# Optimization experiments

Measured on AMD Instinct MI355X. Metric: run time of the kernel, lower is better.

The kernel has to match this reference:

```python
import jax, jax.numpy as jnp
import numpy as np

N_NODES = 50000
N_GRAPHS = 512
HIDDEN = 128
BN_EPS = 1e-5


def setup_inputs() -> dict:
    key = jax.random.key(0)
    ks = jax.random.split(key, 16)
    E = 800000
    x = jax.random.normal(ks[0], (N_NODES, 1), dtype=jnp.float32)
    pos = jax.random.normal(ks[1], (N_NODES, 3), dtype=jnp.float32)
    edge_index = jax.random.randint(ks[2], (2, E), 0, N_NODES, dtype=jnp.int64)
    batch = jnp.sort(jax.random.randint(ks[3], (N_NODES,), 0, N_GRAPHS, dtype=jnp.int64))

    def lin(k, fan_in, fan_out):
        bound = 1.0 / np.sqrt(fan_in)
        return jax.random.uniform(k, (fan_in, fan_out), jnp.float32, -bound, bound)

    # conv1: in=1 -> concat dim 2*1+3=5
    c1_w1 = lin(ks[4], 5, HIDDEN); c1_b1 = jnp.zeros((HIDDEN,), jnp.float32)
    c1_w2 = lin(ks[5], HIDDEN, HIDDEN); c1_b2 = jnp.zeros((HIDDEN,), jnp.float32)
    # conv2: in=128 -> concat dim 2*128+3=259
    c2_w1 = lin(ks[6], 2 * HIDDEN + 3, HIDDEN); c2_b1 = jnp.zeros((HIDDEN,), jnp.float32)
    c2_w2 = lin(ks[7], HIDDEN, HIDDEN); c2_b2 = jnp.zeros((HIDDEN,), jnp.float32)
    # predictor MLP [128, 128, 1], bias=[False, True], batch_norm + relu between
    p_w1 = lin(ks[8], HIDDEN, HIDDEN)
    bn_gamma = jnp.ones((HIDDEN,), jnp.float32)
    bn_beta = jnp.zeros((HIDDEN,), jnp.float32)
    p_w2 = lin(ks[9], HIDDEN, 1)
    p_b2 = jnp.zeros((1,), jnp.float32)
    return {
        "x": x, "pos": pos, "edge_index": edge_index, "batch": batch,
        "c1_w1": c1_w1, "c1_b1": c1_b1, "c1_w2": c1_w2, "c1_b2": c1_b2,
        "c2_w1": c2_w1, "c2_b1": c2_b1, "c2_w2": c2_w2, "c2_b2": c2_b2,
        "p_w1": p_w1, "bn_gamma": bn_gamma, "bn_beta": bn_beta,
        "p_w2": p_w2, "p_b2": p_b2,
    }


def _conv(x, pos, src, dst, w1, b1, w2, b2):
    # gather endpoints; PyG: x_j = x[src], x_i = x[dst], aggregate into dst
    feat = jnp.concatenate([x[dst], x[src], pos[src] - pos[dst]], axis=-1)  # [E, 2F+3]
    msg = jax.nn.relu(feat @ w1 + b1) @ w2 + b2  # [E, H]
    return jax.ops.segment_sum(msg, dst, num_segments=N_NODES)  # [N, H]


def reference(x, pos, edge_index, batch,
              c1_w1, c1_b1, c1_w2, c1_b2,
              c2_w1, c2_b1, c2_w2, c2_b2,
              p_w1, bn_gamma, bn_beta, p_w2, p_b2):
    src, dst = edge_index[0], edge_index[1]
    h = jax.nn.relu(_conv(x, pos, src, dst, c1_w1, c1_b1, c1_w2, c1_b2))
    h = jax.nn.relu(_conv(h, pos, src, dst, c2_w1, c2_b1, c2_w2, c2_b2))
    g = jax.ops.segment_sum(h, batch, num_segments=N_GRAPHS)  # [G, H] global add pool
    # predictor: Linear(no bias) -> BatchNorm(train stats) -> ReLU -> Linear(bias)
    z = g @ p_w1
    mean = jnp.mean(z, axis=0)
    var = jnp.var(z, axis=0)
    z = bn_gamma * (z - mean) * jax.lax.rsqrt(var + BN_EPS) + bn_beta
    z = jax.nn.relu(z)
    return z @ p_w2 + p_b2  # [G, 1]
```

## Files before the change

### kernel.cpp

```cpp
#include <hip/hip_runtime.h>
#include <hip/hip_bf16.h>

#define HID 128
#define DMAX 64

typedef unsigned int uint;
typedef unsigned short ushort;
using short8 = __attribute__((ext_vector_type(8))) short;
using f32x4  = __attribute__((ext_vector_type(4))) float;

#define MFMA_B16(a, b, c) __builtin_amdgcn_mfma_f32_16x16x32_bf16(a, b, c, 0, 0, 0)

__device__ inline ushort bf16rn(float f) {
  uint u = __float_as_uint(f);
  u += 0x7fff + ((u >> 16) & 1);
  return (ushort)(u >> 16);
}
__device__ inline uint packbf(float a, float b) {
  return (uint)bf16rn(a) | ((uint)bf16rn(b) << 16);
}
__device__ inline float bflo(uint u) { return __uint_as_float(u << 16); }
__device__ inline float bfhi(uint u) { return __uint_as_float(u & 0xffff0000u); }

__global__ __launch_bounds__(256) void k_prep(
    const float* __restrict__ x, const float* __restrict__ pos,
    const float* __restrict__ c1w2, const float* __restrict__ c2w1, const float* __restrict__ c2w2,
    float4* __restrict__ xp, int* __restrict__ deg, float* __restrict__ g,
    ushort* __restrict__ w1t, ushort* __restrict__ wdt,
    ushort* __restrict__ wst, ushort* __restrict__ w2t,
    int N, int G, int Npad) {
  int idx = blockIdx.x * 256 + threadIdx.x;
  if (idx < Npad) deg[idx] = 0;
  if (idx < G * HID) g[idx] = 0.f;
  if (idx < N) {
    xp[idx] = make_float4(pos[3 * idx], pos[3 * idx + 1], pos[3 * idx + 2], x[idx]);
  }
  {
    int m = idx >> 14, e = idx & 16383;
    int c = e >> 7, k = e & 127;
    const float* src;
    ushort* dst;
    if (m == 0)      { src = c1w2;              dst = w1t; }
    else if (m == 1) { src = c2w1;              dst = wdt; }
    else if (m == 2) { src = c2w1 + 128 * 128;  dst = wst; }
    else             { src = c2w2;              dst = w2t; }
    dst[e] = bf16rn(src[k * 128 + c]);
  }
}

__global__ void k_build(const int* __restrict__ dstv, const int* __restrict__ srcv,
                        int* __restrict__ deg, int* __restrict__ srcsP, int E) {
  int e = blockIdx.x * 256 + threadIdx.x;
  if (e < E) {
    int d = dstv[e];
    int r = atomicAdd(&deg[d], 1);
    if (r < DMAX) srcsP[(size_t)d * DMAX + r] = srcv[e];
  }
}

__global__ __launch_bounds__(64) void k_conv1(
    const float4* __restrict__ xp,
    const int* __restrict__ deg, const int* __restrict__ srcsP,
    const float* __restrict__ w1, const float* __restrict__ b1, uint* __restrict__ hs) {
  int n = blockIdx.x;
  int lane = threadIdx.x;
  int f0 = 2 * lane;
  __shared__ float sxs[64];
  __shared__ float sdp[3][64];
  int cnt = min(deg[n], DMAX);
  float4 me = xp[n];
  float xi = me.w;
  float2 a1 = *(const float2*)&w1[HID + f0];
  float2 a2 = *(const float2*)&w1[2 * HID + f0];
  float2 a3 = *(const float2*)&w1[3 * HID + f0];
  float2 a4 = *(const float2*)&w1[4 * HID + f0];
  float c_0 = fmaf(xi, w1[f0],     b1[f0]);
  float c_1 = fmaf(xi, w1[f0 + 1], b1[f0 + 1]);
  float acc0 = 0.f, acc1 = 0.f;
  if (lane < cnt) {
    int s = srcsP[(size_t)n * DMAX + lane];
    float4 v = xp[s];
    sxs[lane] = v.w;
    sdp[0][lane] = v.x - me.x;
    sdp[1][lane] = v.y - me.y;
    sdp[2][lane] = v.z - me.z;
  }
  __syncthreads();
  for (int k = 0; k < cnt; ++k) {
    float xj = sxs[k], d0 = sdp[0][k], d1 = sdp[1][k], d2 = sdp[2][k];
    float h0 = fmaf(xj, a1.x, fmaf(d0, a2.x, fmaf(d1, a3.x, fmaf(d2, a4.x, c_0))));
    float h1 = fmaf(xj, a1.y, fmaf(d0, a2.y, fmaf(d1, a3.y, fmaf(d2, a4.y, c_1))));
    acc0 += fmaxf(h0, 0.f);
    acc1 += fmaxf(h1, 0.f);
  }
  hs[(size_t)n * 64 + lane] = packbf(acc0, acc1);
}

__global__ __launch_bounds__(64) void k_conv2(
    const float4* __restrict__ xp,
    const int* __restrict__ deg, const int* __restrict__ srcsP,
    const float* __restrict__ pd, const uint* __restrict__ ps,
    const float* __restrict__ wc, uint* __restrict__ hs) {
  int n = blockIdx.x;
  int lane = threadIdx.x;
  int eg = lane >> 4;
  int fb = lane & 15;
  int f0 = 8 * fb;
  __shared__ int ssrc[64];
  __shared__ float sdp[3][64];
  int cnt = min(deg[n], DMAX);
  float4 me = xp[n];
  float c0[8], c1[8], c2[8], pdv[8], acc[8];
  #pragma unroll
  for (int i = 0; i < 8; ++i) {
    c0[i]  = wc[f0 + i];
    c1[i]  = wc[HID + f0 + i];
    c2[i]  = wc[2 * HID + f0 + i];
    pdv[i] = pd[(size_t)n * HID + f0 + i];
    acc[i] = 0.f;
  }
  if (lane < cnt) {
    int s = srcsP[(size_t)n * DMAX + lane];
    float4 v = xp[s];
    ssrc[lane] = s;
    sdp[0][lane] = v.x - me.x;
    sdp[1][lane] = v.y - me.y;
    sdp[2][lane] = v.z - me.z;
  }
  __syncthreads();
  for (int k = 0; k < cnt; k += 16) {
    int ke[4] = {k + eg, k + 4 + eg, k + 8 + eg, k + 12 + eg};
    int kc[4];
    #pragma unroll
    for (int j = 0; j < 4; ++j) kc[j] = min(ke[j], cnt - 1);
    int se[4] = {ssrc[kc[0]], ssrc[kc[1]], ssrc[kc[2]], ssrc[kc[3]]};
    uint4 u[4];
    #pragma unroll
    for (int j = 0; j < 4; ++j) u[j] = *(const uint4*)&ps[(size_t)se[j] * 64 + fb * 4];
    #pragma unroll
    for (int j = 0; j < 4; ++j) {
      float d0 = sdp[0][kc[j]], d1 = sdp[1][kc[j]], d2 = sdp[2][kc[j]];
      bool vv = ke[j] < cnt;
      uint uu[4] = {u[j].x, u[j].y, u[j].z, u[j].w};
      if (vv) {
        #pragma unroll
        for (int q = 0; q < 4; ++q) {
          float w0  = pdv[2*q]   + fmaf(d0, c0[2*q],   fmaf(d1, c1[2*q],   d2 * c2[2*q]));
          float w1v = pdv[2*q+1] + fmaf(d0, c0[2*q+1], fmaf(d1, c1[2*q+1], d2 * c2[2*q+1]));
          acc[2*q]   += fmaxf(w0  + bflo(uu[q]), 0.f);
          acc[2*q+1] += fmaxf(w1v + bfhi(uu[q]), 0.f);
        }
      }
    }
  }
  #pragma unroll
  for (int i = 0; i < 8; ++i) {
    acc[i] += __shfl_xor(acc[i], 16);
    acc[i] += __shfl_xor(acc[i], 32);
  }
  if (eg == 0) {
    uint4 o;
    o.x = packbf(acc[0], acc[1]);
    o.y = packbf(acc[2], acc[3]);
    o.z = packbf(acc[4], acc[5]);
    o.w = packbf(acc[6], acc[7]);
    *(uint4*)&hs[(size_t)n * 64 + fb * 4] = o;
  }
}

template <int MODE>
__global__ __launch_bounds__(256) void k_mgemm(
    const ushort* __restrict__ A, const ushort* __restrict__ Wt, const ushort* __restrict__ Wt2,
    const float* __restrict__ bias, const int* __restrict__ deg, const int* __restrict__ batch,
    uint* __restrict__ Obf, float* __restrict__ Of, int M) {
  int t = threadIdx.x;
  int l = t & 63;
  int rl = l & 15, kg = l >> 4;
  int r = blockIdx.x * 64 + (t >> 6) * 16 + rl;
  int rc = min(r, M - 1);
  bool valid = (r < M);
  const short8* arow = (const short8*)(A + (size_t)rc * 128);
  short8 af0 = arow[kg], af1 = arow[4 + kg], af2 = arow[8 + kg], af3 = arow[12 + kg];
  float dg = 0.f;
  int bt = 0, gf = 0, gl = 0;
  if (MODE == 0 || MODE == 2) dg = valid ? (float)deg[r] : 0.f;
  if (MODE == 2) {
    bt = batch[rc];
    gf = __shfl(bt, 0);
    gl = __shfl(bt, 15);
  }
  #pragma unroll
  for (int nt = 0; nt < 8; ++nt) {
    const short8* wrow = (const short8*)(Wt + (size_t)(nt * 16 + rl) * 128);
    f32x4 acc = {0.f, 0.f, 0.f, 0.f};
    acc = MFMA_B16(wrow[kg],      af0, acc);
    acc = MFMA_B16(wrow[4 + kg],  af1, acc);
    acc = MFMA_B16(wrow[8 + kg],  af2, acc);
    acc = MFMA_B16(wrow[12 + kg], af3, acc);
    int c0 = nt * 16 + kg * 4;
    if (MODE == 0) {
      f32x4 b4 = *(const f32x4*)&bias[c0];
      float v0 = fmaxf(fmaf(dg, b4[0], acc[0]), 0.f);
      float v1 = fmaxf(fmaf(dg, b4[1], acc[1]), 0.f);
      float v2 = fmaxf(fmaf(dg, b4[2], acc[2]), 0.f);
      float v3 = fmaxf(fmaf(dg, b4[3], acc[3]), 0.f);
      if (valid) {
        uint2 o = {packbf(v0, v1), packbf(v2, v3)};
        *(uint2*)&Obf[(size_t)r * 64 + (c0 >> 1)] = o;
      }
    } else if (MODE == 1) {
      const short8* w2row = (const short8*)(Wt2 + (size_t)(nt * 16 + rl) * 128);
      f32x4 acc2 = {0.f, 0.f, 0.f, 0.f};
      acc2 = MFMA_B16(w2row[kg],      af0, acc2);
      acc2 = MFMA_B16(w2row[4 + kg],  af1, acc2);
      acc2 = MFMA_B16(w2row[8 + kg],  af2, acc2);
      acc2 = MFMA_B16(w2row[12 + kg], af3, acc2);
      if (valid) {
        f32x4 b4 = *(const f32x4*)&bias[c0];
        f32x4 pdv = {acc[0] + b4[0], acc[1] + b4[1], acc[2] + b4[2], acc[3] + b4[3]};
        *(f32x4*)&Of[(size_t)r * 128 + c0] = pdv;
        uint2 o = {packbf(acc2[0], acc2[1]), packbf(acc2[2], acc2[3])};
        *(uint2*)&Obf[(size_t)r * 64 + (c0 >> 1)] = o;
      }
    } else {
      f32x4 b4 = *(const f32x4*)&bias[c0];
      float v0 = valid ? fmaxf(fmaf(dg, b4[0], acc[0]), 0.f) : 0.f;
      float v1 = valid ? fmaxf(fmaf(dg, b4[1], acc[1]), 0.f) : 0.f;
      float v2 = valid ? fmaxf(fmaf(dg, b4[2], acc[2]), 0.f) : 0.f;
      float v3 = valid ? fmaxf(fmaf(dg, b4[3], acc[3]), 0.f) : 0.f;
      for (int gg = gf; gg <= gl; ++gg) {
        bool mine = (bt == gg);
        float s0 = mine ? v0 : 0.f;
        float s1 = mine ? v1 : 0.f;
        float s2 = mine ? v2 : 0.f;
        float s3 = mine ? v3 : 0.f;
        #pragma unroll
        for (int m = 1; m <= 8; m <<= 1) {
          s0 += __shfl_xor(s0, m);
          s1 += __shfl_xor(s1, m);
          s2 += __shfl_xor(s2, m);
          s3 += __shfl_xor(s3, m);
        }
        if (rl == 0) {
          float* gp = &Of[(size_t)gg * 128 + c0];
          atomicAdd(gp + 0, s0);
          atomicAdd(gp + 1, s1);
          atomicAdd(gp + 2, s2);
          atomicAdd(gp + 3, s3);
        }
      }
    }
  }
}

__global__ __launch_bounds__(256) void k_pgemm(
    const float* __restrict__ A, const float* __restrict__ W, float* __restrict__ O1, int M) {
  __shared__ float As[128][36];
  int t = threadIdx.x;
  int n0 = blockIdx.x * 32;
  int j = t & 127, m = t >> 7;
  for (int idx = t; idx < 32 * 128; idx += 256) {
    int r = idx >> 7, i = idx & 127;
    int n = n0 + r;
    As[i][r] = (n < M) ? A[(size_t)n * 128 + i] : 0.f;
  }
  __syncthreads();
  float acc[16];
  #pragma unroll
  for (int r = 0; r < 16; ++r) acc[r] = 0.f;
  int rb = m * 16;
  for (int i = 0; i < 128; ++i) {
    float w = W[i * 128 + j];
    const float4* ap = reinterpret_cast<const float4*>(&As[i][rb]);
    #pragma unroll
    for (int q = 0; q < 4; ++q) {
      float4 a = ap[q];
      acc[q * 4 + 0] = fmaf(a.x, w, acc[q * 4 + 0]);
      acc[q * 4 + 1] = fmaf(a.y, w, acc[q * 4 + 1]);
      acc[q * 4 + 2] = fmaf(a.z, w, acc[q * 4 + 2]);
      acc[q * 4 + 3] = fmaf(a.w, w, acc[q * 4 + 3]);
    }
  }
  #pragma unroll
  for (int r = 0; r < 16; ++r) {
    int n = n0 + rb + r;
    if (n < M) O1[(size_t)n * 128 + j] = acc[r];
  }
}

__global__ __launch_bounds__(256) void k_bn2(const float* __restrict__ z,
                                             float* __restrict__ mv, int G) {
  int j = blockIdx.x;
  int t = threadIdx.x;
  float v1 = (t < G) ? z[(size_t)t * 128 + j] : 0.f;
  float v2 = (t + 256 < G) ? z[(size_t)(t + 256) * 128 + j] : 0.f;
  float s = v1 + v2;
  float q = fmaf(v1, v1, v2 * v2);
  #pragma unroll
  for (int off = 32; off; off >>= 1) {
    s += __shfl_down(s, off);
    q += __shfl_down(q, off);
  }
  __shared__ float ws[4], wq[4];
  int wid = t >> 6, lane = t & 63;
  if (lane == 0) { ws[wid] = s; wq[wid] = q; }
  __syncthreads();
  if (t == 0) {
    float S = ws[0] + ws[1] + ws[2] + ws[3];
    float Q = wq[0] + wq[1] + wq[2] + wq[3];
    float mean = S / (float)G;
    float var = Q / (float)G - mean * mean;
    mv[j] = mean;
    mv[128 + j] = rsqrtf(var + 1e-5f);
  }
}

__global__ __launch_bounds__(256) void k_final(
    const float* __restrict__ z, const float* __restrict__ mv,
    const float* __restrict__ gamma, const float* __restrict__ beta,
    const float* __restrict__ w2, const float* __restrict__ b2,
    float* __restrict__ out, int G) {
  int wid = threadIdx.x >> 6, lane = threadIdx.x & 63;
  int r = blockIdx.x * 4 + wid;
  if (r >= G) return;
  float acc = 0.f;
  #pragma unroll
  for (int h = 0; h < 2; ++h) {
    int jj = lane + h * 64;
    float v = z[(size_t)r * 128 + jj];
    float zn = fmaf((v - mv[jj]) * mv[128 + jj], gamma[jj], beta[jj]);
    acc = fmaf(fmaxf(zn, 0.f), w2[jj], acc);
  }
  #pragma unroll
  for (int off = 32; off; off >>= 1) acc += __shfl_down(acc, off);
  if (lane == 0) out[r] = acc + b2[0];
}

extern "C" void kernel_launch(void* const* d_in, const int* in_sizes, int n_in,
                              void* d_out, int out_size, void* d_ws, size_t ws_size,
                              hipStream_t stream) {
  const float* x     = (const float*)d_in[0];
  const float* pos   = (const float*)d_in[1];
  const int*   eidx  = (const int*)d_in[2];
  const int*   batch = (const int*)d_in[3];
  const float* c1w1  = (const float*)d_in[4];
  const float* c1b1  = (const float*)d_in[5];
  const float* c1w2  = (const float*)d_in[6];
  const float* c1b2  = (const float*)d_in[7];
  const float* c2w1  = (const float*)d_in[8];
  const float* c2b1  = (const float*)d_in[9];
  const float* c2w2  = (const float*)d_in[10];
  const float* c2b2  = (const float*)d_in[11];
  const float* pw1   = (const float*)d_in[12];
  const float* gamma = (const float*)d_in[13];
  const float* beta  = (const float*)d_in[14];
  const float* pw2   = (const float*)d_in[15];
  const float* pb2   = (const float*)d_in[16];
  (void)n_in; (void)ws_size;

  const int N = in_sizes[0];
  const int E = in_sizes[2] / 2;
  const int G = out_size;
  const int* srcv = eidx;
  const int* dstv = eidx + E;

  char* w = (char*)d_ws;
  size_t o = 0;
  auto carve = [&](size_t bytes) { void* p = w + o; o = (o + bytes + 255) & ~(size_t)255; return p; };
  int Npad = ((N + 255) / 256) * 256;
  int* deg    = (int*)carve((size_t)Npad * 4);
  int* srcsP  = (int*)carve((size_t)N * DMAX * 4);
  float4* xp  = (float4*)carve((size_t)N * 16);
  uint*   hs1  = (uint*)carve((size_t)N * 64 * 4);
  ushort* h1   = (ushort*)carve((size_t)N * 128 * 2);
  float*  pdf  = (float*)carve((size_t)N * 128 * 4);
  uint*   psb  = (uint*)carve((size_t)N * 64 * 4);
  uint*   hs2  = (uint*)carve((size_t)N * 64 * 4);
  ushort* w1t  = (ushort*)carve(16384 * 2);
  ushort* wdt  = (ushort*)carve(16384 * 2);
  ushort* wst  = (ushort*)carve(16384 * 2);
  ushort* w2t  = (ushort*)carve(16384 * 2);
  float* g    = (float*)carve((size_t)G * HID * 4);
  float* z    = (float*)carve((size_t)G * HID * 4);
  float* mv   = (float*)carve(256 * 4);

  int nbE = (E + 255) / 256;

  k_prep<<<256, 256, 0, stream>>>(x, pos, c1w2, c2w1, c2w2,
                                  xp, deg, g, w1t, wdt, wst, w2t, N, G, Npad);
  k_build<<<nbE, 256, 0, stream>>>(dstv, srcv, deg, srcsP, E);

  int gb = (N + 63) / 64;
  k_conv1<<<N, 64, 0, stream>>>(xp, deg, srcsP, c1w1, c1b1, hs1);
  k_mgemm<0><<<gb, 256, 0, stream>>>((const ushort*)hs1, w1t, nullptr, c1b2, deg, nullptr,
                                     (uint*)h1, nullptr, N);
  k_mgemm<1><<<gb, 256, 0, stream>>>(h1, wdt, wst, c2b1, nullptr, nullptr,
                                     psb, pdf, N);
  k_conv2<<<N, 64, 0, stream>>>(xp, deg, srcsP, pdf, psb, c2w1 + 256 * HID, hs2);
  k_mgemm<2><<<gb, 256, 0, stream>>>((const ushort*)hs2, w2t, nullptr, c2b2, deg, batch,
                                     nullptr, g, N);
  k_pgemm<<<(G + 31) / 32, 256, 0, stream>>>(g, pw1, z, G);
  k_bn2<<<HID, 256, 0, stream>>>(z, mv, G);
  k_final<<<(G + 3) / 4, 256, 0, stream>>>(z, mv, gamma, beta, pw2, pb2, (float*)d_out, G);
}
```

Measured before the change: 206.7 us.

## Split degree atomics into two parity buckets and store pd as bf16

Edges are split by index parity into two counter arrays and two 32-slot halves of each adjacency row. This halves atomic contention on popular destination nodes during the CSR build. The conv2 precomputed dst-term is now written and read as bf16 rather than fp32, cutting that buffer's traffic. The changes add precision loss on pd, and each half now overflows separately at 32 entries instead of the row overflowing at 64.

```diff
diff --git a/kernel.cpp b/kernel.cpp
--- a/kernel.cpp
+++ b/kernel.cpp
@@ -3,6 +3,7 @@
 
 #define HID 128
 #define DMAX 64
+#define BCAP 32
 
 typedef unsigned int uint;
 typedef unsigned short ushort;
@@ -25,12 +26,15 @@
 __global__ __launch_bounds__(256) void k_prep(
     const float* __restrict__ x, const float* __restrict__ pos,
     const float* __restrict__ c1w2, const float* __restrict__ c2w1, const float* __restrict__ c2w2,
-    float4* __restrict__ xp, int* __restrict__ deg, float* __restrict__ g,
+    float4* __restrict__ xp, int* __restrict__ deg2, float* __restrict__ g,
     ushort* __restrict__ w1t, ushort* __restrict__ wdt,
     ushort* __restrict__ wst, ushort* __restrict__ w2t,
     int N, int G, int Npad) {
   int idx = blockIdx.x * 256 + threadIdx.x;
-  if (idx < Npad) deg[idx] = 0;
+  if (idx < Npad) {
+    deg2[idx] = 0;
+    deg2[Npad + idx] = 0;
+  }
   if (idx < G * HID) g[idx] = 0.f;
   if (idx < N) {
     xp[idx] = make_float4(pos[3 * idx], pos[3 * idx + 1], pos[3 * idx + 2], x[idx]);
@@ -49,25 +53,28 @@
 }
 
 __global__ void k_build(const int* __restrict__ dstv, const int* __restrict__ srcv,
-                        int* __restrict__ deg, int* __restrict__ srcsP, int E) {
+                        int* __restrict__ deg2, int* __restrict__ srcsP, int E, int Npad) {
   int e = blockIdx.x * 256 + threadIdx.x;
   if (e < E) {
     int d = dstv[e];
-    int r = atomicAdd(&deg[d], 1);
-    if (r < DMAX) srcsP[(size_t)d * DMAX + r] = srcv[e];
+    int b = e & 1;
+    int r = atomicAdd(&deg2[(size_t)b * Npad + d], 1);
+    if (r < BCAP) srcsP[(size_t)d * DMAX + b * BCAP + r] = srcv[e];
   }
 }
 
 __global__ __launch_bounds__(64) void k_conv1(
     const float4* __restrict__ xp,
-    const int* __restrict__ deg, const int* __restrict__ srcsP,
-    const float* __restrict__ w1, const float* __restrict__ b1, uint* __restrict__ hs) {
+    const int* __restrict__ deg2, const int* __restrict__ srcsP,
+    const float* __restrict__ w1, const float* __restrict__ b1, uint* __restrict__ hs,
+    int Npad) {
   int n = blockIdx.x;
   int lane = threadIdx.x;
   int f0 = 2 * lane;
   __shared__ float sxs[64];
   __shared__ float sdp[3][64];
-  int cnt = min(deg[n], DMAX);
+  int d0 = min(deg2[n], BCAP);
+  int d1 = min(deg2[Npad + n], BCAP);
   float4 me = xp[n];
   float xi = me.w;
   float2 a1 = *(const float2*)&w1[HID + f0];
@@ -77,7 +84,8 @@
   float c_0 = fmaf(xi, w1[f0],     b1[f0]);
   float c_1 = fmaf(xi, w1[f0 + 1], b1[f0 + 1]);
   float acc0 = 0.f, acc1 = 0.f;
-  if (lane < cnt) {
+  bool valid = (lane < BCAP) ? (lane < d0) : (lane - BCAP < d1);
+  if (valid) {
     int s = srcsP[(size_t)n * DMAX + lane];
     float4 v = xp[s];
     sxs[lane] = v.w;
@@ -86,21 +94,26 @@
     sdp[2][lane] = v.z - me.z;
   }
   __syncthreads();
-  for (int k = 0; k < cnt; ++k) {
-    float xj = sxs[k], d0 = sdp[0][k], d1 = sdp[1][k], d2 = sdp[2][k];
-    float h0 = fmaf(xj, a1.x, fmaf(d0, a2.x, fmaf(d1, a3.x, fmaf(d2, a4.x, c_0))));
-    float h1 = fmaf(xj, a1.y, fmaf(d0, a2.y, fmaf(d1, a3.y, fmaf(d2, a4.y, c_1))));
-    acc0 += fmaxf(h0, 0.f);
-    acc1 += fmaxf(h1, 0.f);
+  #pragma unroll
+  for (int seg = 0; seg < 2; ++seg) {
+    int kb = seg * BCAP;
+    int kcnt = seg ? d1 : d0;
+    for (int k = kb; k < kb + kcnt; ++k) {
+      float xj = sxs[k], d0v = sdp[0][k], d1v = sdp[1][k], d2v = sdp[2][k];
+      float h0 = fmaf(xj, a1.x, fmaf(d0v, a2.x, fmaf(d1v, a3.x, fmaf(d2v, a4.x, c_0))));
+      float h1 = fmaf(xj, a1.y, fmaf(d0v, a2.y, fmaf(d1v, a3.y, fmaf(d2v, a4.y, c_1))));
+      acc0 += fmaxf(h0, 0.f);
+      acc1 += fmaxf(h1, 0.f);
+    }
   }
   hs[(size_t)n * 64 + lane] = packbf(acc0, acc1);
 }
 
 __global__ __launch_bounds__(64) void k_conv2(
     const float4* __restrict__ xp,
-    const int* __restrict__ deg, const int* __restrict__ srcsP,
-    const float* __restrict__ pd, const uint* __restrict__ ps,
-    const float* __restrict__ wc, uint* __restrict__ hs) {
+    const int* __restrict__ deg2, const int* __restrict__ srcsP,
+    const uint* __restrict__ pdb, const uint* __restrict__ ps,
+    const float* __restrict__ wc, uint* __restrict__ hs, int Npad) {
   int n = blockIdx.x;
   int lane = threadIdx.x;
   int eg = lane >> 4;
@@ -108,18 +121,26 @@
   int f0 = 8 * fb;
   __shared__ int ssrc[64];
   __shared__ float sdp[3][64];
-  int cnt = min(deg[n], DMAX);
+  int d0 = min(deg2[n], BCAP);
+  int d1 = min(deg2[Npad + n], BCAP);
   float4 me = xp[n];
   float c0[8], c1[8], c2[8], pdv[8], acc[8];
+  uint4 pdu = *(const uint4*)&pdb[(size_t)n * 64 + fb * 4];
+  uint pdua[4] = {pdu.x, pdu.y, pdu.z, pdu.w};
+  #pragma unroll
+  for (int i = 0; i < 4; ++i) {
+    pdv[2 * i]     = bflo(pdua[i]);
+    pdv[2 * i + 1] = bfhi(pdua[i]);
+  }
   #pragma unroll
   for (int i = 0; i < 8; ++i) {
     c0[i]  = wc[f0 + i];
     c1[i]  = wc[HID + f0 + i];
     c2[i]  = wc[2 * HID + f0 + i];
-    pdv[i] = pd[(size_t)n * HID + f0 + i];
     acc[i] = 0.f;
   }
-  if (lane < cnt) {
+  bool validl = (lane < BCAP) ? (lane < d0) : (lane - BCAP < d1);
+  if (validl) {
     int s = srcsP[(size_t)n * DMAX + lane];
     float4 v = xp[s];
     ssrc[lane] = s;
@@ -128,27 +149,32 @@
     sdp[2][lane] = v.z - me.z;
   }
   __syncthreads();
-  for (int k = 0; k < cnt; k += 16) {
-    int ke[4] = {k + eg, k + 4 + eg, k + 8 + eg, k + 12 + eg};
-    int kc[4];
-    #pragma unroll
-    for (int j = 0; j < 4; ++j) kc[j] = min(ke[j], cnt - 1);
-    int se[4] = {ssrc[kc[0]], ssrc[kc[1]], ssrc[kc[2]], ssrc[kc[3]]};
-    uint4 u[4];
-    #pragma unroll
-    for (int j = 0; j < 4; ++j) u[j] = *(const uint4*)&ps[(size_t)se[j] * 64 + fb * 4];
-    #pragma unroll
-    for (int j = 0; j < 4; ++j) {
-      float d0 = sdp[0][kc[j]], d1 = sdp[1][kc[j]], d2 = sdp[2][kc[j]];
-      bool vv = ke[j] < cnt;
-      uint uu[4] = {u[j].x, u[j].y, u[j].z, u[j].w};
-      if (vv) {
-        #pragma unroll
-        for (int q = 0; q < 4; ++q) {
-          float w0  = pdv[2*q]   + fmaf(d0, c0[2*q],   fmaf(d1, c1[2*q],   d2 * c2[2*q]));
-          float w1v = pdv[2*q+1] + fmaf(d0, c0[2*q+1], fmaf(d1, c1[2*q+1], d2 * c2[2*q+1]));
-          acc[2*q]   += fmaxf(w0  + bflo(uu[q]), 0.f);
-          acc[2*q+1] += fmaxf(w1v + bfhi(uu[q]), 0.f);
+  #pragma unroll
+  for (int seg = 0; seg < 2; ++seg) {
+    int kb = seg * BCAP;
+    int cnt = seg ? d1 : d0;
+    for (int k = 0; k < cnt; k += 16) {
+      int ke[4] = {k + eg, k + 4 + eg, k + 8 + eg, k + 12 + eg};
+      int kc[4];
+      #pragma unroll
+      for (int j = 0; j < 4; ++j) kc[j] = kb + min(ke[j], cnt - 1);
+      int se[4] = {ssrc[kc[0]], ssrc[kc[1]], ssrc[kc[2]], ssrc[kc[3]]};
+      uint4 u[4];
+      #pragma unroll
+      for (int j = 0; j < 4; ++j) u[j] = *(const uint4*)&ps[(size_t)se[j] * 64 + fb * 4];
+      #pragma unroll
+      for (int j = 0; j < 4; ++j) {
+        float dd0 = sdp[0][kc[j]], dd1 = sdp[1][kc[j]], dd2 = sdp[2][kc[j]];
+        bool vv = ke[j] < cnt;
+        uint uu[4] = {u[j].x, u[j].y, u[j].z, u[j].w};
+        if (vv) {
+          #pragma unroll
+          for (int q = 0; q < 4; ++q) {
+            float w0  = pdv[2*q]   + fmaf(dd0, c0[2*q],   fmaf(dd1, c1[2*q],   dd2 * c2[2*q]));
+            float w1v = pdv[2*q+1] + fmaf(dd0, c0[2*q+1], fmaf(dd1, c1[2*q+1], dd2 * c2[2*q+1]));
+            acc[2*q]   += fmaxf(w0  + bflo(uu[q]), 0.f);
+            acc[2*q+1] += fmaxf(w1v + bfhi(uu[q]), 0.f);
+          }
         }
       }
     }
@@ -171,8 +197,8 @@
 template <int MODE>
 __global__ __launch_bounds__(256) void k_mgemm(
     const ushort* __restrict__ A, const ushort* __restrict__ Wt, const ushort* __restrict__ Wt2,
-    const float* __restrict__ bias, const int* __restrict__ deg, const int* __restrict__ batch,
-    uint* __restrict__ Obf, float* __restrict__ Of, int M) {
+    const float* __restrict__ bias, const int* __restrict__ deg2, const int* __restrict__ batch,
+    uint* __restrict__ Obf, uint* __restrict__ Obf2, float* __restrict__ Of, int M, int Npad) {
   int t = threadIdx.x;
   int l = t & 63;
   int rl = l & 15, kg = l >> 4;
@@ -183,7 +209,7 @@
   short8 af0 = arow[kg], af1 = arow[4 + kg], af2 = arow[8 + kg], af3 = arow[12 + kg];
   float dg = 0.f;
   int bt = 0, gf = 0, gl = 0;
-  if (MODE == 0 || MODE == 2) dg = valid ? (float)deg[r] : 0.f;
+  if (MODE == 0 || MODE == 2) dg = valid ? (float)(deg2[r] + deg2[Npad + r]) : 0.f;
   if (MODE == 2) {
     bt = batch[rc];
     gf = __shfl(bt, 0);
@@ -217,10 +243,11 @@
       acc2 = MFMA_B16(w2row[12 + kg], af3, acc2);
       if (valid) {
         f32x4 b4 = *(const f32x4*)&bias[c0];
-        f32x4 pdv = {acc[0] + b4[0], acc[1] + b4[1], acc[2] + b4[2], acc[3] + b4[3]};
-        *(f32x4*)&Of[(size_t)r * 128 + c0] = pdv;
-        uint2 o = {packbf(acc2[0], acc2[1]), packbf(acc2[2], acc2[3])};
-        *(uint2*)&Obf[(size_t)r * 64 + (c0 >> 1)] = o;
+        uint2 opd = {packbf(acc[0] + b4[0], acc[1] + b4[1]),
+                     packbf(acc[2] + b4[2], acc[3] + b4[3])};
+        *(uint2*)&Obf2[(size_t)r * 64 + (c0 >> 1)] = opd;
+        uint2 ops = {packbf(acc2[0], acc2[1]), packbf(acc2[2], acc2[3])};
+        *(uint2*)&Obf[(size_t)r * 64 + (c0 >> 1)] = ops;
       }
     } else {
       f32x4 b4 = *(const f32x4*)&bias[c0];
@@ -368,12 +395,12 @@
   size_t o = 0;
   auto carve = [&](size_t bytes) { void* p = w + o; o = (o + bytes + 255) & ~(size_t)255; return p; };
   int Npad = ((N + 255) / 256) * 256;
-  int* deg    = (int*)carve((size_t)Npad * 4);
+  int* deg2   = (int*)carve((size_t)2 * Npad * 4);
   int* srcsP  = (int*)carve((size_t)N * DMAX * 4);
   float4* xp  = (float4*)carve((size_t)N * 16);
   uint*   hs1  = (uint*)carve((size_t)N * 64 * 4);
   ushort* h1   = (ushort*)carve((size_t)N * 128 * 2);
-  float*  pdf  = (float*)carve((size_t)N * 128 * 4);
+  uint*   pdb  = (uint*)carve((size_t)N * 64 * 4);
   uint*   psb  = (uint*)carve((size_t)N * 64 * 4);
   uint*   hs2  = (uint*)carve((size_t)N * 64 * 4);
   ushort* w1t  = (ushort*)carve(16384 * 2);
@@ -387,18 +414,18 @@
   int nbE = (E + 255) / 256;
 
   k_prep<<<256, 256, 0, stream>>>(x, pos, c1w2, c2w1, c2w2,
-                                  xp, deg, g, w1t, wdt, wst, w2t, N, G, Npad);
-  k_build<<<nbE, 256, 0, stream>>>(dstv, srcv, deg, srcsP, E);
+                                  xp, deg2, g, w1t, wdt, wst, w2t, N, G, Npad);
+  k_build<<<nbE, 256, 0, stream>>>(dstv, srcv, deg2, srcsP, E, Npad);
 
   int gb = (N + 63) / 64;
-  k_conv1<<<N, 64, 0, stream>>>(xp, deg, srcsP, c1w1, c1b1, hs1);
-  k_mgemm<0><<<gb, 256, 0, stream>>>((const ushort*)hs1, w1t, nullptr, c1b2, deg, nullptr,
-                                     (uint*)h1, nullptr, N);
+  k_conv1<<<N, 64, 0, stream>>>(xp, deg2, srcsP, c1w1, c1b1, hs1, Npad);
+  k_mgemm<0><<<gb, 256, 0, stream>>>((const ushort*)hs1, w1t, nullptr, c1b2, deg2, nullptr,
+                                     (uint*)h1, nullptr, nullptr, N, Npad);
   k_mgemm<1><<<gb, 256, 0, stream>>>(h1, wdt, wst, c2b1, nullptr, nullptr,
-                                     psb, pdf, N);
-  k_conv2<<<N, 64, 0, stream>>>(xp, deg, srcsP, pdf, psb, c2w1 + 256 * HID, hs2);
-  k_mgemm<2><<<gb, 256, 0, stream>>>((const ushort*)hs2, w2t, nullptr, c2b2, deg, batch,
-                                     nullptr, g, N);
+                                     psb, pdb, nullptr, N, Npad);
+  k_conv2<<<N, 64, 0, stream>>>(xp, deg2, srcsP, pdb, psb, c2w1 + 256 * HID, hs2, Npad);
+  k_mgemm<2><<<gb, 256, 0, stream>>>((const ushort*)hs2, w2t, nullptr, c2b2, deg2, batch,
+                                     nullptr, nullptr, g, N, Npad);
   k_pgemm<<<(G + 31) / 32, 256, 0, stream>>>(g, pw1, z, G);
   k_bn2<<<HID, 256, 0, stream>>>(z, mv, G);
   k_final<<<(G + 3) / 4, 256, 0, stream>>>(z, mv, gamma, beta, pw2, pb2, (float*)d_out, G);
```

New measurement: 211.1 us. 2.1% more time.

## Fuse conv1 output GEMM with conv2 projections and pad degree counters

Applied to the files above, without the earlier changes.

Merges the conv1 second-layer GEMM and the conv2 first-layer projections into one kernel that keeps the intermediate activations in LDS, removing a global round-trip and a launch. The dst-side projection is now stored as bf16 instead of fp32, halving its traffic at some precision cost. Degree counters are spread to one per 128-byte line to reduce atomic contention, at the cost of a larger buffer to zero and scattered degree reads.

```diff
diff --git a/kernel.cpp b/kernel.cpp
--- a/kernel.cpp
+++ b/kernel.cpp
@@ -3,6 +3,7 @@
 
 #define HID 128
 #define DMAX 64
+#define DSTRIDE 32
 
 typedef unsigned int uint;
 typedef unsigned short ushort;
@@ -25,12 +26,13 @@
 __global__ __launch_bounds__(256) void k_prep(
     const float* __restrict__ x, const float* __restrict__ pos,
     const float* __restrict__ c1w2, const float* __restrict__ c2w1, const float* __restrict__ c2w2,
-    float4* __restrict__ xp, int* __restrict__ deg, float* __restrict__ g,
+    float4* __restrict__ xp, int* __restrict__ degP, float* __restrict__ g,
     ushort* __restrict__ w1t, ushort* __restrict__ wdt,
     ushort* __restrict__ wst, ushort* __restrict__ w2t,
     int N, int G, int Npad) {
   int idx = blockIdx.x * 256 + threadIdx.x;
-  if (idx < Npad) deg[idx] = 0;
+  int stride = gridDim.x * 256;
+  for (int i = idx; i < Npad * DSTRIDE; i += stride) degP[i] = 0;
   if (idx < G * HID) g[idx] = 0.f;
   if (idx < N) {
     xp[idx] = make_float4(pos[3 * idx], pos[3 * idx + 1], pos[3 * idx + 2], x[idx]);
@@ -49,25 +51,25 @@
 }
 
 __global__ void k_build(const int* __restrict__ dstv, const int* __restrict__ srcv,
-                        int* __restrict__ deg, int* __restrict__ srcsP, int E) {
+                        int* __restrict__ degP, int* __restrict__ srcsP, int E) {
   int e = blockIdx.x * 256 + threadIdx.x;
   if (e < E) {
     int d = dstv[e];
-    int r = atomicAdd(&deg[d], 1);
+    int r = atomicAdd(&degP[(size_t)d * DSTRIDE], 1);
     if (r < DMAX) srcsP[(size_t)d * DMAX + r] = srcv[e];
   }
 }
 
 __global__ __launch_bounds__(64) void k_conv1(
     const float4* __restrict__ xp,
-    const int* __restrict__ deg, const int* __restrict__ srcsP,
+    const int* __restrict__ degP, const int* __restrict__ srcsP,
     const float* __restrict__ w1, const float* __restrict__ b1, uint* __restrict__ hs) {
   int n = blockIdx.x;
   int lane = threadIdx.x;
   int f0 = 2 * lane;
   __shared__ float sxs[64];
   __shared__ float sdp[3][64];
-  int cnt = min(deg[n], DMAX);
+  int cnt = min(degP[(size_t)n * DSTRIDE], DMAX);
   float4 me = xp[n];
   float xi = me.w;
   float2 a1 = *(const float2*)&w1[HID + f0];
@@ -96,10 +98,75 @@
   hs[(size_t)n * 64 + lane] = packbf(acc0, acc1);
 }
 
+__global__ __launch_bounds__(256) void k_mfuse(
+    const ushort* __restrict__ A, const ushort* __restrict__ W1t,
+    const ushort* __restrict__ Wdt, const ushort* __restrict__ Wst,
+    const float* __restrict__ b1, const float* __restrict__ bd,
+    const int* __restrict__ degP,
+    uint* __restrict__ psb, uint* __restrict__ pdb, int M) {
+  __shared__ uint hl[64][68];
+  int t = threadIdx.x;
+  int l = t & 63;
+  int rl = l & 15, kg = l >> 4, wv = t >> 6;
+  int rloc = wv * 16 + rl;
+  int r = blockIdx.x * 64 + rloc;
+  int rc = min(r, M - 1);
+  bool valid = (r < M);
+  const short8* arow = (const short8*)(A + (size_t)rc * 128);
+  short8 af0 = arow[kg], af1 = arow[4 + kg], af2 = arow[8 + kg], af3 = arow[12 + kg];
+  float dg = valid ? (float)degP[(size_t)r * DSTRIDE] : 0.f;
+  #pragma unroll
+  for (int nt = 0; nt < 8; ++nt) {
+    const short8* wrow = (const short8*)(W1t + (size_t)(nt * 16 + rl) * 128);
+    f32x4 acc = {0.f, 0.f, 0.f, 0.f};
+    acc = MFMA_B16(wrow[kg],      af0, acc);
+    acc = MFMA_B16(wrow[4 + kg],  af1, acc);
+    acc = MFMA_B16(wrow[8 + kg],  af2, acc);
+    acc = MFMA_B16(wrow[12 + kg], af3, acc);
+    int c0 = nt * 16 + kg * 4;
+    f32x4 b4 = *(const f32x4*)&b1[c0];
+    float v0 = fmaxf(fmaf(dg, b4[0], acc[0]), 0.f);
+    float v1 = fmaxf(fmaf(dg, b4[1], acc[1]), 0.f);
+    float v2 = fmaxf(fmaf(dg, b4[2], acc[2]), 0.f);
+    float v3 = fmaxf(fmaf(dg, b4[3], acc[3]), 0.f);
+    hl[rloc][(c0 >> 1)]     = packbf(v0, v1);
+    hl[rloc][(c0 >> 1) + 1] = packbf(v2, v3);
+  }
+  __syncthreads();
+  const uint* hrow = hl[rloc];
+  short8 bfrag[4];
+  #pragma unroll
+  for (int i = 0; i < 4; ++i) bfrag[i] = *(const short8*)&hrow[i * 16 + kg * 4];
+  #pragma unroll
+  for (int nt = 0; nt < 8; ++nt) {
+    const short8* wsrow = (const short8*)(Wst + (size_t)(nt * 16 + rl) * 128);
+    const short8* wdrow = (const short8*)(Wdt + (size_t)(nt * 16 + rl) * 128);
+    f32x4 accS = {0.f, 0.f, 0.f, 0.f};
+    f32x4 accD = {0.f, 0.f, 0.f, 0.f};
+    accS = MFMA_B16(wsrow[kg],      bfrag[0], accS);
+    accS = MFMA_B16(wsrow[4 + kg],  bfrag[1], accS);
+    accS = MFMA_B16(wsrow[8 + kg],  bfrag[2], accS);
+    accS = MFMA_B16(wsrow[12 + kg], bfrag[3], accS);
+    accD = MFMA_B16(wdrow[kg],      bfrag[0], accD);
+    accD = MFMA_B16(wdrow[4 + kg],  bfrag[1], accD);
+    accD = MFMA_B16(wdrow[8 + kg],  bfrag[2], accD);
+    accD = MFMA_B16(wdrow[12 + kg], bfrag[3], accD);
+    int c0 = nt * 16 + kg * 4;
+    if (valid) {
+      f32x4 b4 = *(const f32x4*)&bd[c0];
+      uint2 opd = {packbf(accD[0] + b4[0], accD[1] + b4[1]),
+                   packbf(accD[2] + b4[2], accD[3] + b4[3])};
+      *(uint2*)&pdb[(size_t)r * 64 + (c0 >> 1)] = opd;
+      uint2 ops = {packbf(accS[0], accS[1]), packbf(accS[2], accS[3])};
+      *(uint2*)&psb[(size_t)r * 64 + (c0 >> 1)] = ops;
+    }
+  }
+}
+
 __global__ __launch_bounds__(64) void k_conv2(
     const float4* __restrict__ xp,
-    const int* __restrict__ deg, const int* __restrict__ srcsP,
-    const float* __restrict__ pd, const uint* __restrict__ ps,
+    const int* __restrict__ degP, const int* __restrict__ srcsP,
+    const uint* __restrict__ pdb, const uint* __restrict__ ps,
     const float* __restrict__ wc, uint* __restrict__ hs) {
   int n = blockIdx.x;
   int lane = threadIdx.x;
@@ -108,15 +175,21 @@
   int f0 = 8 * fb;
   __shared__ int ssrc[64];
   __shared__ float sdp[3][64];
-  int cnt = min(deg[n], DMAX);
+  int cnt = min(degP[(size_t)n * DSTRIDE], DMAX);
   float4 me = xp[n];
   float c0[8], c1[8], c2[8], pdv[8], acc[8];
+  uint4 pdu = *(const uint4*)&pdb[(size_t)n * 64 + fb * 4];
+  uint pdua[4] = {pdu.x, pdu.y, pdu.z, pdu.w};
+  #pragma unroll
+  for (int i = 0; i < 4; ++i) {
+    pdv[2 * i]     = bflo(pdua[i]);
+    pdv[2 * i + 1] = bfhi(pdua[i]);
+  }
   #pragma unroll
   for (int i = 0; i < 8; ++i) {
     c0[i]  = wc[f0 + i];
     c1[i]  = wc[HID + f0 + i];
     c2[i]  = wc[2 * HID + f0 + i];
-    pdv[i] = pd[(size_t)n * HID + f0 + i];
     acc[i] = 0.f;
   }
   if (lane < cnt) {
@@ -139,14 +212,14 @@
     for (int j = 0; j < 4; ++j) u[j] = *(const uint4*)&ps[(size_t)se[j] * 64 + fb * 4];
     #pragma unroll
     for (int j = 0; j < 4; ++j) {
-      float d0 = sdp[0][kc[j]], d1 = sdp[1][kc[j]], d2 = sdp[2][kc[j]];
+      float dd0 = sdp[0][kc[j]], dd1 = sdp[1][kc[j]], dd2 = sdp[2][kc[j]];
       bool vv = ke[j] < cnt;
       uint uu[4] = {u[j].x, u[j].y, u[j].z, u[j].w};
       if (vv) {
         #pragma unroll
         for (int q = 0; q < 4; ++q) {
-          float w0  = pdv[2*q]   + fmaf(d0, c0[2*q],   fmaf(d1, c1[2*q],   d2 * c2[2*q]));
-          float w1v = pdv[2*q+1] + fmaf(d0, c0[2*q+1], fmaf(d1, c1[2*q+1], d2 * c2[2*q+1]));
+          float w0  = pdv[2*q]   + fmaf(dd0, c0[2*q],   fmaf(dd1, c1[2*q],   dd2 * c2[2*q]));
+          float w1v = pdv[2*q+1] + fmaf(dd0, c0[2*q+1], fmaf(dd1, c1[2*q+1], dd2 * c2[2*q+1]));
           acc[2*q]   += fmaxf(w0  + bflo(uu[q]), 0.f);
           acc[2*q+1] += fmaxf(w1v + bfhi(uu[q]), 0.f);
         }
@@ -168,11 +241,10 @@
   }
 }
 
-template <int MODE>
-__global__ __launch_bounds__(256) void k_mgemm(
-    const ushort* __restrict__ A, const ushort* __restrict__ Wt, const ushort* __restrict__ Wt2,
-    const float* __restrict__ bias, const int* __restrict__ deg, const int* __restrict__ batch,
-    uint* __restrict__ Obf, float* __restrict__ Of, int M) {
+__global__ __launch_bounds__(256) void k_mpool(
+    const ushort* __restrict__ A, const ushort* __restrict__ Wt,
+    const float* __restrict__ bias, const int* __restrict__ degP, const int* __restrict__ batch,
+    float* __restrict__ Of, int M) {
   int t = threadIdx.x;
   int l = t & 63;
   int rl = l & 15, kg = l >> 4;
@@ -181,14 +253,10 @@
   bool valid = (r < M);
   const short8* arow = (const short8*)(A + (size_t)rc * 128);
   short8 af0 = arow[kg], af1 = arow[4 + kg], af2 = arow[8 + kg], af3 = arow[12 + kg];
-  float dg = 0.f;
-  int bt = 0, gf = 0, gl = 0;
-  if (MODE == 0 || MODE == 2) dg = valid ? (float)deg[r] : 0.f;
-  if (MODE == 2) {
-    bt = batch[rc];
-    gf = __shfl(bt, 0);
-    gl = __shfl(bt, 15);
-  }
+  float dg = valid ? (float)degP[(size_t)r * DSTRIDE] : 0.f;
+  int bt = batch[rc];
+  int gf = __shfl(bt, 0);
+  int gl = __shfl(bt, 15);
   #pragma unroll
   for (int nt = 0; nt < 8; ++nt) {
     const short8* wrow = (const short8*)(Wt + (size_t)(nt * 16 + rl) * 128);
@@ -198,56 +266,30 @@
     acc = MFMA_B16(wrow[8 + kg],  af2, acc);
     acc = MFMA_B16(wrow[12 + kg], af3, acc);
     int c0 = nt * 16 + kg * 4;
-    if (MODE == 0) {
-      f32x4 b4 = *(const f32x4*)&bias[c0];
-      float v0 = fmaxf(fmaf(dg, b4[0], acc[0]), 0.f);
-      float v1 = fmaxf(fmaf(dg, b4[1], acc[1]), 0.f);
-      float v2 = fmaxf(fmaf(dg, b4[2], acc[2]), 0.f);
-      float v3 = fmaxf(fmaf(dg, b4[3], acc[3]), 0.f);
-      if (valid) {
-        uint2 o = {packbf(v0, v1), packbf(v2, v3)};
-        *(uint2*)&Obf[(size_t)r * 64 + (c0 >> 1)] = o;
+    f32x4 b4 = *(const f32x4*)&bias[c0];
+    float v0 = valid ? fmaxf(fmaf(dg, b4[0], acc[0]), 0.f) : 0.f;
+    float v1 = valid ? fmaxf(fmaf(dg, b4[1], acc[1]), 0.f) : 0.f;
+    float v2 = valid ? fmaxf(fmaf(dg, b4[2], acc[2]), 0.f) : 0.f;
+    float v3 = valid ? fmaxf(fmaf(dg, b4[3], acc[3]), 0.f) : 0.f;
+    for (int gg = gf; gg <= gl; ++gg) {
+      bool mine = (bt == gg);
+      float s0 = mine ? v0 : 0.f;
+      float s1 = mine ? v1 : 0.f;
+      float s2 = mine ? v2 : 0.f;
+      float s3 = mine ? v3 : 0.f;
+      #pragma unroll
+      for (int m = 1; m <= 8; m <<= 1) {
+        s0 += __shfl_xor(s0, m);
+        s1 += __shfl_xor(s1, m);
+        s2 += __shfl_xor(s2, m);
+        s3 += __shfl_xor(s3, m);
       }
-    } else if (MODE == 1) {
-      const short8* w2row = (const short8*)(Wt2 + (size_t)(nt * 16 + rl) * 128);
-      f32x4 acc2 = {0.f, 0.f, 0.f, 0.f};
-      acc2 = MFMA_B16(w2row[kg],      af0, acc2);
-      acc2 = MFMA_B16(w2row[4 + kg],  af1, acc2);
-      acc2 = MFMA_B16(w2row[8 + kg],  af2, acc2);
-      acc2 = MFMA_B16(w2row[12 + kg], af3, acc2);
-      if (valid) {
-        f32x4 b4 = *(const f32x4*)&bias[c0];
-        f32x4 pdv = {acc[0] + b4[0], acc[1] + b4[1], acc[2] + b4[2], acc[3] + b4[3]};
-        *(f32x4*)&Of[(size_t)r * 128 + c0] = pdv;
-        uint2 o = {packbf(acc2[0], acc2[1]), packbf(acc2[2], acc2[3])};
-        *(uint2*)&Obf[(size_t)r * 64 + (c0 >> 1)] = o;
-      }
-    } else {
-      f32x4 b4 = *(const f32x4*)&bias[c0];
-      float v0 = valid ? fmaxf(fmaf(dg, b4[0], acc[0]), 0.f) : 0.f;
-      float v1 = valid ? fmaxf(fmaf(dg, b4[1], acc[1]), 0.f) : 0.f;
-      float v2 = valid ? fmaxf(fmaf(dg, b4[2], acc[2]), 0.f) : 0.f;
-      float v3 = valid ? fmaxf(fmaf(dg, b4[3], acc[3]), 0.f) : 0.f;
-      for (int gg = gf; gg <= gl; ++gg) {
-        bool mine = (bt == gg);
-        float s0 = mine ? v0 : 0.f;
-        float s1 = mine ? v1 : 0.f;
-        float s2 = mine ? v2 : 0.f;
-        float s3 = mine ? v3 : 0.f;
-        #pragma unroll
-        for (int m = 1; m <= 8; m <<= 1) {
-          s0 += __shfl_xor(s0, m);
-          s1 += __shfl_xor(s1, m);
-          s2 += __shfl_xor(s2, m);
-          s3 += __shfl_xor(s3, m);
-        }
-        if (rl == 0) {
-          float* gp = &Of[(size_t)gg * 128 + c0];
-          atomicAdd(gp + 0, s0);
-          atomicAdd(gp + 1, s1);
-          atomicAdd(gp + 2, s2);
-          atomicAdd(gp + 3, s3);
-        }
+      if (rl == 0) {
+        float* gp = &Of[(size_t)gg * 128 + c0];
+        atomicAdd(gp + 0, s0);
+        atomicAdd(gp + 1, s1);
+        atomicAdd(gp + 2, s2);
+        atomicAdd(gp + 3, s3);
       }
     }
   }
@@ -368,12 +410,11 @@
   size_t o = 0;
   auto carve = [&](size_t bytes) { void* p = w + o; o = (o + bytes + 255) & ~(size_t)255; return p; };
   int Npad = ((N + 255) / 256) * 256;
-  int* deg    = (int*)carve((size_t)Npad * 4);
+  int* degP   = (int*)carve((size_t)Npad * DSTRIDE * 4);
   int* srcsP  = (int*)carve((size_t)N * DMAX * 4);
   float4* xp  = (float4*)carve((size_t)N * 16);
   uint*   hs1  = (uint*)carve((size_t)N * 64 * 4);
-  ushort* h1   = (ushort*)carve((size_t)N * 128 * 2);
-  float*  pdf  = (float*)carve((size_t)N * 128 * 4);
+  uint*   pdb  = (uint*)carve((size_t)N * 64 * 4);
   uint*   psb  = (uint*)carve((size_t)N * 64 * 4);
   uint*   hs2  = (uint*)carve((size_t)N * 64 * 4);
   ushort* w1t  = (ushort*)carve(16384 * 2);
@@ -387,18 +428,15 @@
   int nbE = (E + 255) / 256;
 
   k_prep<<<256, 256, 0, stream>>>(x, pos, c1w2, c2w1, c2w2,
-                                  xp, deg, g, w1t, wdt, wst, w2t, N, G, Npad);
-  k_build<<<nbE, 256, 0, stream>>>(dstv, srcv, deg, srcsP, E);
+                                  xp, degP, g, w1t, wdt, wst, w2t, N, G, Npad);
+  k_build<<<nbE, 256, 0, stream>>>(dstv, srcv, degP, srcsP, E);
 
   int gb = (N + 63) / 64;
-  k_conv1<<<N, 64, 0, stream>>>(xp, deg, srcsP, c1w1, c1b1, hs1);
-  k_mgemm<0><<<gb, 256, 0, stream>>>((const ushort*)hs1, w1t, nullptr, c1b2, deg, nullptr,
-                                     (uint*)h1, nullptr, N);
-  k_mgemm<1><<<gb, 256, 0, stream>>>(h1, wdt, wst, c2b1, nullptr, nullptr,
-                                     psb, pdf, N);
-  k_conv2<<<N, 64, 0, stream>>>(xp, deg, srcsP, pdf, psb, c2w1 + 256 * HID, hs2);
-  k_mgemm<2><<<gb, 256, 0, stream>>>((const ushort*)hs2, w2t, nullptr, c2b2, deg, batch,
-                                     nullptr, g, N);
+  k_conv1<<<N, 64, 0, stream>>>(xp, degP, srcsP, c1w1, c1b1, hs1);
+  k_mfuse<<<gb, 256, 0, stream>>>((const ushort*)hs1, w1t, wdt, wst, c1b2, c2b1, degP,
+                                  psb, pdb, N);
+  k_conv2<<<N, 64, 0, stream>>>(xp, degP, srcsP, pdb, psb, c2w1 + 256 * HID, hs2);
+  k_mpool<<<gb, 256, 0, stream>>>((const ushort*)hs2, w2t, c2b2, degP, batch, g, N);
   k_pgemm<<<(G + 31) / 32, 256, 0, stream>>>(g, pw1, z, G);
   k_bn2<<<HID, 256, 0, stream>>>(z, mv, G);
   k_final<<<(G + 3) / 4, 256, 0, stream>>>(z, mv, gamma, beta, pw2, pb2, (float*)d_out, G);
```

Result: no change. 205.7 us (-0.5%).
